# Kernel tuning notes

Hardware: AMD Instinct MI355X
Metric: run time of the kernel (lower is better)

Reference implementation:

```python
import jax, jax.numpy as jnp
import numpy as np
from jax import lax

TAU = 2.0
EPS = 1e-5
STEP = 10      # time steps
RATIO = 4     # TIM_ratio
HEADS = 16
SCALE = 0.25


@jax.custom_vjp
def _spike(v):
    return (v > 0.0).astype(v.dtype)

def _spike_fwd(v):
    return _spike(v), v

def _spike_bwd(v, g):
    alpha = 4.0  # sigmoid surrogate gradient
    s = jax.nn.sigmoid(alpha * v)
    return (g * alpha * s * (1.0 - s),)

_spike.defvjp(_spike_fwd, _spike_bwd)


def lif(x, vth=1.0):
    """LIF neuron over leading time dim: mem += (x-mem)/tau, fire, hard reset (detached)."""
    def step(mem, xt):
        mem = mem + (xt - mem) / TAU
        s = _spike(mem - vth)
        mem = mem * (1.0 - lax.stop_gradient(s))
        return mem, s
    _, out = lax.scan(step, jnp.zeros_like(x[0]), x)
    return out


def bn(x, p, axis):
    """Inference-mode batchnorm; p = stacked (gamma, beta, mean, var) along dim 0."""
    g, b, m, v = p
    sh = [1] * x.ndim
    sh[axis] = -1
    return (x - m.reshape(sh)) / jnp.sqrt(v.reshape(sh) + EPS) * g.reshape(sh) + b.reshape(sh)


def conv3d(x, w, groups=1):
    return lax.conv_general_dilated(
        x, w, window_strides=(1, 1, 1), padding=[(1, 1)] * 3,
        dimension_numbers=('NCDHW', 'OIDHW', 'NCDHW'),
        feature_group_count=groups)


def tim(x, up_w, bn1, down_w, bn2):
    # x: (T, B, C, H, W); conv3d treats T as channels, (C,H,W) as the volume
    T, B, C, H, W = x.shape
    y = conv3d(jnp.swapaxes(x, 0, 1), up_w)                      # (B, T*R, C, H, W)
    y = jnp.swapaxes(bn(y, bn1, 1), 0, 1)                        # (T*R, B, C, H, W)
    # MyNode reshapes (T*R*B, ...) into STEP time chunks of size R*B
    y = lif(y.reshape(STEP, -1, C, H, W)).reshape(T * RATIO, B, C, H, W)
    y = conv3d(jnp.swapaxes(y, 0, 1), down_w, groups=STEP)       # (B, T, C, H, W)
    y = jnp.swapaxes(bn(y, bn2, 1), 0, 1)                        # (T, B, C, H, W)
    return lif(y)


def ssa(x, q_w, q_bn, k_w, k_bn, v_w, v_bn, proj_w, proj_bn,
        tim_up_w, tim_bn1, tim_down_w, tim_bn2):
    T, B, C, H, W = x.shape
    N = H * W
    d = C // HEADS
    xf = x.reshape(T * B, C, N)

    def branch(w, bnp):
        y = bn(jnp.einsum('oc,bcn->bon', w, xf), bnp, 1).reshape(T, B, C, H, W)
        y = tim(y, tim_up_w, tim_bn1, tim_down_w, tim_bn2)       # binary spikes
        y = y.reshape(T, B, C, N).transpose(0, 1, 3, 2)          # (T, B, N, C)
        return y.reshape(T, B, N, HEADS, d).transpose(0, 1, 3, 2, 4)  # (T, B, h, N, d)

    q = branch(q_w, q_bn)
    k = branch(k_w, k_bn)
    v = branch(v_w, v_bn)
    attn = jnp.einsum('tbhnd,tbhmd->tbhnm', q, k)                # no softmax (spiking attn)
    o = jnp.einsum('tbhnm,tbhmd->tbhnd', attn, v) * SCALE
    o = o.transpose(0, 1, 2, 4, 3).reshape(T, B, C, N)           # merge (h, d) -> C
    o = lif(o, vth=0.5)                                          # attn_lif, threshold 0.5
    o = bn(jnp.einsum('oc,tbcn->tbon', proj_w, o), proj_bn, 2)   # 1x1 conv1d + BN1d
    return lif(o).reshape(T, B, C, H, W)


def mlp(x, fc1_w, fc1_b, fc1_bn, fc2_w, fc2_b, fc2_bn):
    T, B, C, H, W = x.shape
    y = jnp.einsum('oc,tbchw->tbohw', fc1_w, x) + fc1_b.reshape(1, 1, -1, 1, 1)
    y = lif(bn(y, fc1_bn, 2))
    y = jnp.einsum('oc,tbchw->tbohw', fc2_w, y) + fc2_b.reshape(1, 1, -1, 1, 1)
    return lif(bn(y, fc2_bn, 2))


def setup_inputs() -> dict:
    key = jax.random.key(0)
    ks = jax.random.split(key, 24)
    T, B, C, H, W = 10, 4, 256, 16, 16
    HID = 1024

    def bnp(k, c):
        k1, k2, k3, k4 = jax.random.split(k, 4)
        gamma = jax.random.uniform(k1, (c,), minval=0.5, maxval=1.5)
        beta = 0.1 * jax.random.normal(k2, (c,))
        mean = 0.1 * jax.random.normal(k3, (c,))
        var = jax.random.uniform(k4, (c,), minval=0.5, maxval=1.5)
        return jnp.stack([gamma, beta, mean, var]).astype(jnp.float32)

    inp = {
        'x': jax.random.normal(ks[0], (T, B, C, H, W), jnp.float32),
        'q_w': jax.random.normal(ks[1], (C, C)) / np.sqrt(C),
        'q_bn': bnp(ks[2], C),
        'k_w': jax.random.normal(ks[3], (C, C)) / np.sqrt(C),
        'k_bn': bnp(ks[4], C),
        'v_w': jax.random.normal(ks[5], (C, C)) / np.sqrt(C),
        'v_bn': bnp(ks[6], C),
        'proj_w': jax.random.normal(ks[7], (C, C)) / np.sqrt(C),
        'proj_bn': bnp(ks[8], C),
        'tim_up_w': jax.random.normal(ks[9], (STEP * RATIO, STEP, 3, 3, 3)) / np.sqrt(STEP * 27),
        'tim_bn1': bnp(ks[10], STEP * RATIO),
        'tim_down_w': jax.random.normal(ks[11], (STEP, RATIO, 3, 3, 3)) / np.sqrt(RATIO * 27),
        'tim_bn2': bnp(ks[12], STEP),
        'fc1_w': jax.random.normal(ks[13], (HID, C)) / np.sqrt(C),
        'fc1_b': 0.1 * jax.random.normal(ks[14], (HID,)),
        'fc1_bn': bnp(ks[15], HID),
        'fc2_w': jax.random.normal(ks[16], (C, HID)) / np.sqrt(HID),
        'fc2_b': 0.1 * jax.random.normal(ks[17], (C,)),
        'fc2_bn': bnp(ks[18], C),
    }
    return {k: v.astype(jnp.float32) for k, v in inp.items()}


def reference(x, q_w, q_bn, k_w, k_bn, v_w, v_bn, proj_w, proj_bn,
              tim_up_w, tim_bn1, tim_down_w, tim_bn2,
              fc1_w, fc1_b, fc1_bn, fc2_w, fc2_b, fc2_bn):
    h = x + ssa(x, q_w, q_bn, k_w, k_bn, v_w, v_bn, proj_w, proj_bn,
                tim_up_w, tim_bn1, tim_down_w, tim_bn2)
    return h + mlp(h, fc1_w, fc1_b, fc1_bn, fc2_w, fc2_b, fc2_bn)
```

## Files before the change

kernel.cpp:

```cpp
#include <hip/hip_runtime.h>
#include <cstdint>
#include <cstddef>

#define EPSF 1e-5f

typedef __attribute__((ext_vector_type(8))) short short8;
typedef __attribute__((ext_vector_type(4))) float f32x4;

__device__ __forceinline__ unsigned short bf16_rne(float f) {
    unsigned int u = __float_as_uint(f);
    u += 0x7FFFu + ((u >> 16) & 1u);
    return (unsigned short)(u >> 16);
}
__device__ __forceinline__ float bf16f(unsigned short h) {
    return __uint_as_float(((unsigned int)h) << 16);
}

__device__ __forceinline__ void split_pack_body(
    const float* __restrict__ W, unsigned short* __restrict__ P,
    int O, int K, int idx)
{
    const int OT = O >> 4, KT = K >> 5;
    const int lane = idx & 63, tile = idx >> 6;
    const int kt = tile % KT, ot = tile / KT;
    const int quad = lane >> 4, l15 = lane & 15;
    const int row = ot * 16 + l15, col = kt * 32 + quad * 8;
    const size_t base = ((size_t)ot * KT + kt) * 512 + lane * 8;
    const size_t sOff = (size_t)OT * KT * 512;
#pragma unroll
    for (int j = 0; j < 8; ++j) {
        float v = W[(size_t)row * K + col + j];
        unsigned short h1 = bf16_rne(v);
        float r = v - bf16f(h1);
        unsigned short h2 = bf16_rne(r);
        float r2 = r - bf16f(h2);
        P[base + j] = h1;
        P[sOff + base + j] = h2;
        P[2 * sOff + base + j] = bf16_rne(r2);
    }
}

__global__ __launch_bounds__(256) void split_pack_k(
    const float* __restrict__ W, unsigned short* __restrict__ P, int O, int K)
{
    int idx = blockIdx.x * 256 + threadIdx.x;
    if (idx >= (O * K) >> 3) return;
    split_pack_body(W, P, O, K, idx);
}

struct SplitArgs { const float* W[3]; unsigned short* P[3]; };
__global__ __launch_bounds__(256) void split_pack3_k(SplitArgs sa, int O, int K)
{
    int idx = blockIdx.x * 256 + threadIdx.x;
    if (idx >= (O * K) >> 3) return;
    split_pack_body(sa.W[blockIdx.y], sa.P[blockIdx.y], O, K, idx);
}

__global__ __launch_bounds__(256) void bpack_k(
    const float* __restrict__ B, unsigned short* __restrict__ BP,
    int K, int N, int S)
{
    const int KT = K >> 5, NT16 = N >> 4;
    int idx = blockIdx.x * 256 + threadIdx.x;
    if (idx >= S * NT16 * KT * 64) return;
    const int lane = idx & 63;
    int tile = idx >> 6;
    const int kt = tile % KT; tile /= KT;
    const int n16 = tile % NT16; const int s = tile / NT16;
    const int quad = lane >> 4, l15 = lane & 15;
    const size_t base = (size_t)idx * 8;
    const size_t sOff = (size_t)S * NT16 * KT * 512;
    const float* src = B + (size_t)s * K * N + (size_t)(kt * 32 + quad * 8) * N
                         + n16 * 16 + l15;
#pragma unroll
    for (int j = 0; j < 8; ++j) {
        float v = src[(size_t)j * N];
        unsigned short h1 = bf16_rne(v);
        float r = v - bf16f(h1);
        unsigned short h2 = bf16_rne(r);
        float r2 = r - bf16f(h2);
        BP[base + j] = h1;
        BP[sOff + base + j] = h2;
        BP[2 * sOff + base + j] = bf16_rne(r2);
    }
}

struct MArgs { const unsigned short* W[3]; float* Out[3]; const float* bn[3]; };

#define MM(AP, BQ)                                                            \
    {                                                                         \
        _Pragma("unroll") for (int mt = 0; mt < 2; ++mt)                      \
        _Pragma("unroll") for (int nt = 0; nt < 2; ++nt)                      \
            acc[mt][nt] = __builtin_amdgcn_mfma_f32_16x16x32_bf16(            \
                Af[AP][mt], Bf[BQ][nt], acc[mt][nt], 0, 0, 0);                \
    }

__global__ __launch_bounds__(256, 4) void mfma_gemm3(
    MArgs a, const unsigned short* __restrict__ BP,
    const float* __restrict__ bias, int O, int K, int N, int nB)
{
    const unsigned short* __restrict__ W = a.W[blockIdx.z];
    float* __restrict__ Out = a.Out[blockIdx.z];
    const float* __restrict__ bnp = a.bn[blockIdx.z];
    const int OT = O >> 4, KT = K >> 5, NT16 = N >> 4;
    const size_t sA = (size_t)OT * KT * 512;
    const size_t sB = (size_t)gridDim.y * NT16 * KT * 512;

    const int slice  = blockIdx.y;
    const int tilesn = N >> 6;
    const int to = (blockIdx.x / tilesn) << 6;
    const int tn = (blockIdx.x % tilesn) << 6;
    const int tid = threadIdx.x;
    const int wid = tid >> 6, lane = tid & 63;
    const int quad = lane >> 4, l15 = lane & 15;
    const int wm = (wid >> 1) << 5, wn = (wid & 1) << 5;
    const int oti0 = (to + wm) >> 4;
    const int n160 = (tn + wn) >> 4;

    f32x4 acc[2][2];
#pragma unroll
    for (int mt = 0; mt < 2; ++mt)
#pragma unroll
        for (int nt = 0; nt < 2; ++nt)
#pragma unroll
            for (int r = 0; r < 4; ++r) acc[mt][nt][r] = 0.0f;

    for (int kt = 0; kt < KT; ++kt) {
        short8 Af[3][2], Bf[3][2];
#pragma unroll
        for (int mt = 0; mt < 2; ++mt) {
            const size_t fa = ((size_t)(oti0 + mt) * KT + kt) * 512 + lane * 8;
            Af[0][mt] = *(const short8*)(W + fa);
            Af[1][mt] = *(const short8*)(W + sA + fa);
            Af[2][mt] = *(const short8*)(W + 2 * sA + fa);
        }
#pragma unroll
        for (int nt = 0; nt < 2; ++nt) {
            const size_t fb =
                (((size_t)slice * NT16 + n160 + nt) * KT + kt) * 512 + lane * 8;
            Bf[0][nt] = *(const short8*)(BP + fb);
            if (nB == 3) {
                Bf[1][nt] = *(const short8*)(BP + sB + fb);
                Bf[2][nt] = *(const short8*)(BP + 2 * sB + fb);
            }
        }
        if (nB == 3) {
            MM(0, 0) MM(0, 1) MM(1, 0) MM(0, 2) MM(1, 1) MM(2, 0)
        } else {
            MM(0, 0) MM(1, 0) MM(2, 0)
        }
    }

    float* Op = Out + (size_t)slice * O * N;
#pragma unroll
    for (int mt = 0; mt < 2; ++mt) {
#pragma unroll
        for (int r = 0; r < 4; ++r) {
            const int o = to + wm + (mt << 4) + (quad << 2) + r;
            float g = bnp[o], bb = bnp[O + o], m = bnp[2 * O + o], vv = bnp[3 * O + o];
            float sq = sqrtf(vv + EPSF);
            float bs = bias ? bias[o] : 0.0f;
#pragma unroll
            for (int nt = 0; nt < 2; ++nt) {
                const int n = tn + wn + (nt << 4) + l15;
                float val = acc[mt][nt][r] + bs;
                Op[(size_t)o * N + n] = (val - m) / sq * g + bb;
            }
        }
    }
}

__global__ __launch_bounds__(256) void wpack6_k(
    const float* __restrict__ up_w, unsigned short* __restrict__ AP)
{
    int idx = blockIdx.x * 256 + threadIdx.x;
    if (idx >= 1920) return;
    const int lane = idx & 63, rest = idx >> 6;
    const int t = rest % 10, mt = rest / 10;
    const int quad = lane >> 4, l15 = lane & 15;
    const int uc = mt * 16 + l15;
    const size_t base = ((size_t)mt * 10 + t) * 512 + lane * 8;
#pragma unroll
    for (int j = 0; j < 8; ++j) {
        int tap = quad * 8 + j;
        float v = 0.0f;
        if (uc < 40 && tap < 27) v = up_w[uc * 270 + t * 27 + tap];
        unsigned short h1 = bf16_rne(v);
        float r = v - bf16f(h1);
        unsigned short h2 = bf16_rne(r);
        float r2 = r - bf16f(h2);
        AP[base + j] = h1;
        AP[15360 + base + j] = h2;
        AP[30720 + base + j] = bf16_rne(r2);
    }
}

struct TimArgs { const float* Y[3]; };

__global__ __launch_bounds__(256, 2) void tim_up6(
    TimArgs ta, const unsigned short* __restrict__ AP,
    const float* __restrict__ bn1, unsigned char* __restrict__ USPK)
{
    __shared__ float smem[12336];
    const float* __restrict__ Y = ta.Y[blockIdx.z];
    unsigned char* __restrict__ SPK = USPK + (size_t)blockIdx.z * 10485760;
    const int c = blockIdx.x, b = blockIdx.y;
    const int tid = threadIdx.x;
    const int wid = tid >> 6, lane = tid & 63;
    const int quad = lane >> 4, l15 = lane & 15;

    int offs[8];
#pragma unroll
    for (int j = 0; j < 8; ++j) {
        int tap = quad * 8 + j;
        if (tap < 27) {
            int kd = tap / 9, rem = tap - kd * 9;
            int kh = rem / 3, kw = rem - kh * 3;
            offs[j] = kd * 360 + kh * 20 + kw;
        } else offs[j] = 0;
    }

    f32x4 acc[3][4];
#pragma unroll
    for (int mt = 0; mt < 3; ++mt)
#pragma unroll
        for (int ng = 0; ng < 4; ++ng)
#pragma unroll
            for (int r = 0; r < 4; ++r) acc[mt][ng][r] = 0.0f;

#pragma unroll 1
    for (int ph = 0; ph < 2; ++ph) {
        __syncthreads();
        for (int idx = tid; idx < 5400; idx += 256) {
            int tt = idx / 1080, rem = idx % 1080;
            int kd = rem / 360, p = rem % 360;
            int row = p / 20, col = p % 20;
            int t = ph * 5 + tt;
            int h = row - 1, ww = col - 1;
            int cs = c + kd - 1;
            float v = 0.0f;
            if (cs >= 0 && cs < 256 && h >= 0 && h < 16 && ww >= 0 && ww < 16)
                v = Y[((t * 4 + b) * 256 + cs) * 256 + h * 16 + ww];
            smem[idx] = v;
        }
        __syncthreads();

#pragma unroll 1
        for (int tt = 0; tt < 5; ++tt) {
            const int t = ph * 5 + tt;
            short8 Af[3][3];
#pragma unroll
            for (int mt = 0; mt < 3; ++mt) {
                const size_t fa = ((size_t)mt * 10 + t) * 512 + lane * 8;
                Af[0][mt] = *(const short8*)(AP + fa);
                Af[1][mt] = *(const short8*)(AP + 15360 + fa);
                Af[2][mt] = *(const short8*)(AP + 30720 + fa);
            }
#pragma unroll
            for (int ng = 0; ng < 4; ++ng) {
                const int base = tt * 1080 + (wid * 4 + ng) * 20 + l15;
                short8 Bf0, Bf1, Bf2;
#pragma unroll
                for (int j = 0; j < 8; ++j) {
                    float v = smem[base + offs[j]];
                    unsigned short h1 = bf16_rne(v);
                    float r = v - bf16f(h1);
                    unsigned short h2 = bf16_rne(r);
                    float r2 = r - bf16f(h2);
                    Bf0[j] = (short)h1;
                    Bf1[j] = (short)h2;
                    Bf2[j] = (short)bf16_rne(r2);
                }
#pragma unroll
                for (int mt = 0; mt < 3; ++mt) {
                    acc[mt][ng] = __builtin_amdgcn_mfma_f32_16x16x32_bf16(
                        Af[0][mt], Bf0, acc[mt][ng], 0, 0, 0);
                    acc[mt][ng] = __builtin_amdgcn_mfma_f32_16x16x32_bf16(
                        Af[0][mt], Bf1, acc[mt][ng], 0, 0, 0);
                    acc[mt][ng] = __builtin_amdgcn_mfma_f32_16x16x32_bf16(
                        Af[1][mt], Bf0, acc[mt][ng], 0, 0, 0);
                    acc[mt][ng] = __builtin_amdgcn_mfma_f32_16x16x32_bf16(
                        Af[0][mt], Bf2, acc[mt][ng], 0, 0, 0);
                    acc[mt][ng] = __builtin_amdgcn_mfma_f32_16x16x32_bf16(
                        Af[1][mt], Bf1, acc[mt][ng], 0, 0, 0);
                    acc[mt][ng] = __builtin_amdgcn_mfma_f32_16x16x32_bf16(
                        Af[2][mt], Bf0, acc[mt][ng], 0, 0, 0);
                }
            }
        }
    }

    __syncthreads();
#pragma unroll
    for (int mt = 0; mt < 3; ++mt)
#pragma unroll
        for (int ng = 0; ng < 4; ++ng)
#pragma unroll
            for (int r = 0; r < 4; ++r) {
                const int uc = mt * 16 + quad * 4 + r;
                const int pix = (wid * 4 + ng) * 16 + l15;
                smem[uc * 257 + pix] = acc[mt][ng][r];
            }
    __syncthreads();

    const int pix = tid;
#pragma unroll
    for (int g = 0; g < 4; ++g) {
        float mem = 0.0f;
#pragma unroll
        for (int s = 0; s < 10; ++s) {
            const int uc = 4 * s + g;
            float ga = bn1[uc], be = bn1[40 + uc], mu = bn1[80 + uc], va = bn1[120 + uc];
            float xv = (smem[uc * 257 + pix] - mu) / sqrtf(va + EPSF) * ga + be;
            mem += (xv - mem) * 0.5f;
            unsigned char spk = mem > 1.0f ? 1 : 0;
            SPK[(((size_t)b * 40 + uc) * 256 + c) * 256 + pix] = spk;
            mem = spk ? 0.0f : mem;
        }
    }
}

struct PtrArgs { float* p[3]; };
struct CPtrArgs { const float* p[3]; };

__global__ __launch_bounds__(256) void tim_down_pre5(
    const unsigned char* __restrict__ USPK, const float* __restrict__ w,
    const float* __restrict__ bn2, PtrArgs PY)
{
    __shared__ float smem[4 * 3 * 324];
    const int br = blockIdx.z / 10, t = blockIdx.z % 10;
    const unsigned char* __restrict__ SPK = USPK + (size_t)br * 10485760;
    float* __restrict__ PreY = PY.p[br];
    const int c = blockIdx.x, b = blockIdx.y;
    const int tid = threadIdx.x;
    for (int idx = tid; idx < 3888; idx += 256) {
        int r = idx / 972, rem = idx % 972;
        int cc = rem / 324, p = rem % 324;
        int hh = p / 18 - 1, ww = p % 18 - 1;
        int cs = c + cc - 1;
        float v = 0.0f;
        if (cs >= 0 && cs < 256 && hh >= 0 && hh < 16 && ww >= 0 && ww < 16)
            v = (float)SPK[(((size_t)b * 40 + 4 * t + r) * 256 + cs) * 256 + hh * 16 + ww];
        smem[idx] = v;
    }
    __syncthreads();
    const int h = tid >> 4, wq = tid & 15;
    float a = 0.0f;
#pragma unroll
    for (int r = 0; r < 4; ++r)
#pragma unroll
        for (int kd = 0; kd < 3; ++kd) {
            const float* wp = w + ((t * 4 + r) * 3 + kd) * 9;
#pragma unroll
            for (int kh = 0; kh < 3; ++kh)
#pragma unroll
                for (int kw = 0; kw < 3; ++kw)
                    a = fmaf(wp[kh * 3 + kw],
                             smem[r * 972 + kd * 324 + (h + kh) * 18 + (wq + kw)], a);
        }
    a = (a - bn2[20 + t]) / sqrtf(bn2[30 + t] + EPSF) * bn2[t] + bn2[10 + t];
    PreY[((t * 4 + b) * 256 + c) * 256 + tid] = a;
}

__global__ __launch_bounds__(256) void lif_down3(CPtrArgs PY, PtrArgs SB)
{
    const float* __restrict__ PreY = PY.p[blockIdx.y];
    float* __restrict__ S = SB.p[blockIdx.y];
    const int idx = blockIdx.x * 256 + threadIdx.x;
    float mem = 0.0f;
    for (int t = 0; t < 10; ++t) {
        float v = PreY[t * 262144 + idx];
        mem += (v - mem) * 0.5f;
        float spk = mem > 1.0f ? 1.0f : 0.0f;
        S[t * 262144 + idx] = spk;
        mem = spk > 0.0f ? 0.0f : mem;
    }
}

__global__ __launch_bounds__(256) void ktv_k(
    const float* __restrict__ SK, const float* __restrict__ SV,
    float* __restrict__ KTV)
{
    __shared__ float ks[16 * 257], vs[16 * 257];
    const int bi = blockIdx.x;
    const int t = bi >> 6, b = (bi >> 4) & 3, hd = bi & 15;
    const int tid = threadIdx.x;
    for (int i = tid; i < 4096; i += 256) {
        int row = i >> 8, col = i & 255;
        ks[row * 257 + col] = SK[((t * 4 + b) * 256 + hd * 16 + row) * 256 + col];
        vs[row * 257 + col] = SV[((t * 4 + b) * 256 + hd * 16 + row) * 256 + col];
    }
    __syncthreads();
    const int j = tid >> 4, j2 = tid & 15;
    float a0 = 0.0f, a1 = 0.0f, a2 = 0.0f, a3 = 0.0f;
#pragma unroll 4
    for (int n = 0; n < 256; n += 4) {
        a0 = fmaf(ks[j * 257 + n + 0], vs[j2 * 257 + n + 0], a0);
        a1 = fmaf(ks[j * 257 + n + 1], vs[j2 * 257 + n + 1], a1);
        a2 = fmaf(ks[j * 257 + n + 2], vs[j2 * 257 + n + 2], a2);
        a3 = fmaf(ks[j * 257 + n + 3], vs[j2 * 257 + n + 3], a3);
    }
    KTV[((t * 4 + b) * 16 + hd) * 256 + tid] = (a0 + a1) + (a2 + a3);
}

__global__ __launch_bounds__(256) void attn_k2(
    const float* __restrict__ SQ, const float* __restrict__ KTV,
    unsigned short* __restrict__ PSPK)
{
    __shared__ float kt[2560];
    __shared__ float qs[16 * 17];
    const int x = blockIdx.x;
    const int b = x >> 8, hd = (x >> 4) & 15, ng = x & 15;
    const int tid = threadIdx.x;
    const int j2 = tid >> 4, nl = tid & 15;
    const int n = ng * 16 + nl;
    for (int i = tid; i < 2560; i += 256) {
        int t = i >> 8;
        kt[i] = KTV[((t * 4 + b) * 16 + hd) * 256 + (i & 255)];
    }
    const int c = hd * 16 + j2;
    const int ktile = c >> 5, quad = (c >> 3) & 3, jj = c & 7;
    const int lane = quad * 16 + nl;
    float mem = 0.0f;
    for (int t = 0; t < 10; ++t) {
        __syncthreads();
        qs[nl * 17 + j2] = SQ[((t * 4 + b) * 256 + hd * 16 + j2) * 256 + n];
        __syncthreads();
        float a = 0.0f;
#pragma unroll
        for (int j = 0; j < 16; ++j)
            a = fmaf(qs[nl * 17 + j], kt[t * 256 + j * 16 + j2], a);
        a *= 0.25f;
        mem += (a - mem) * 0.5f;
        float spk = mem > 0.5f ? 1.0f : 0.0f;
        PSPK[((((size_t)(t * 4 + b) * 16 + ng) * 8 + ktile) * 512) + lane * 8 + jj] =
            spk > 0.0f ? (unsigned short)0x3F80 : (unsigned short)0;
        mem = spk > 0.0f ? 0.0f : mem;
    }
}

__global__ __launch_bounds__(256) void ssa_lif_res(
    const float* __restrict__ P, const float* __restrict__ x,
    float* __restrict__ H)
{
    const int idx = blockIdx.x * 256 + threadIdx.x;
    float mem = 0.0f;
    for (int t = 0; t < 10; ++t) {
        float v = P[t * 262144 + idx];
        mem += (v - mem) * 0.5f;
        float spk = mem > 1.0f ? 1.0f : 0.0f;
        H[t * 262144 + idx] = x[t * 262144 + idx] + spk;
        mem = spk > 0.0f ? 0.0f : mem;
    }
}

__global__ __launch_bounds__(256) void lif_pack(
    const float* __restrict__ A, unsigned short* __restrict__ PB)
{
    const int idx = blockIdx.x * 256 + threadIdx.x;
    const int b = idx >> 18, rem = idx & 262143;
    const int hid = rem >> 8, hw = rem & 255;
    const int ktile = hid >> 5, quad = (hid >> 3) & 3, jj = hid & 7;
    const int n16 = hw >> 4, l15 = hw & 15;
    const int lane = quad * 16 + l15;
    float mem = 0.0f;
    for (int t = 0; t < 10; ++t) {
        float v = A[t * 1048576 + idx];
        mem += (v - mem) * 0.5f;
        float spk = mem > 1.0f ? 1.0f : 0.0f;
        PB[((((size_t)(t * 4 + b) * 16 + n16) * 32 + ktile) * 512) + lane * 8 + jj] =
            spk > 0.0f ? (unsigned short)0x3F80 : (unsigned short)0;
        mem = spk > 0.0f ? 0.0f : mem;
    }
}

__global__ __launch_bounds__(256) void final_k(
    const float* __restrict__ P, const float* __restrict__ H,
    float* __restrict__ out)
{
    const int idx = blockIdx.x * 256 + threadIdx.x;
    float mem = 0.0f;
    for (int t = 0; t < 10; ++t) {
        float v = P[t * 262144 + idx];
        mem += (v - mem) * 0.5f;
        float spk = mem > 1.0f ? 1.0f : 0.0f;
        out[t * 262144 + idx] = H[t * 262144 + idx] + spk;
        mem = spk > 0.0f ? 0.0f : mem;
    }
}

extern "C" void kernel_launch(void* const* d_in, const int* in_sizes, int n_in,
                              void* d_out, int out_size, void* d_ws, size_t ws_size,
                              hipStream_t stream)
{
    const float* x        = (const float*)d_in[0];
    const float* q_w      = (const float*)d_in[1];
    const float* q_bn     = (const float*)d_in[2];
    const float* k_w      = (const float*)d_in[3];
    const float* k_bn     = (const float*)d_in[4];
    const float* v_w      = (const float*)d_in[5];
    const float* v_bn     = (const float*)d_in[6];
    const float* proj_w   = (const float*)d_in[7];
    const float* proj_bn  = (const float*)d_in[8];
    const float* up_w     = (const float*)d_in[9];
    const float* bn1      = (const float*)d_in[10];
    const float* down_w   = (const float*)d_in[11];
    const float* bn2      = (const float*)d_in[12];
    const float* fc1_w    = (const float*)d_in[13];
    const float* fc1_b    = (const float*)d_in[14];
    const float* fc1_bn   = (const float*)d_in[15];
    const float* fc2_w    = (const float*)d_in[16];
    const float* fc2_b    = (const float*)d_in[17];
    const float* fc2_bn   = (const float*)d_in[18];

    float* ws   = (float*)d_ws;
    float* Y    = ws;
    float* ASPK = Y + 2621440;
    float* SQ   = ASPK + 10485760;
    float* SK   = SQ + 2621440;
    float* SV   = SK + 2621440;
    float* KTV  = SV + 2621440;
    unsigned short* AP = (unsigned short*)KTV;

    unsigned short* qs_s = (unsigned short*)ASPK;
    unsigned short* ks_s = qs_s + 196608;
    unsigned short* vs_s = qs_s + 393216;
    unsigned short* xp_s = qs_s + 589824;

    wpack6_k<<<8, 256, 0, stream>>>(up_w, AP);
    SplitArgs sa;
    sa.W[0] = q_w; sa.W[1] = k_w; sa.W[2] = v_w;
    sa.P[0] = qs_s; sa.P[1] = ks_s; sa.P[2] = vs_s;
    split_pack3_k<<<dim3(32, 3), 256, 0, stream>>>(sa, 256, 256);
    bpack_k<<<1280, 256, 0, stream>>>(x, xp_s, 256, 256, 40);

    MArgs qkv;
    qkv.W[0] = qs_s;  qkv.W[1] = ks_s;  qkv.W[2] = vs_s;
    qkv.Out[0] = Y; qkv.Out[1] = SK; qkv.Out[2] = SV;
    qkv.bn[0] = q_bn; qkv.bn[1] = k_bn; qkv.bn[2] = v_bn;
    mfma_gemm3<<<dim3(16, 40, 3), 256, 0, stream>>>(qkv, xp_s, nullptr, 256, 256, 256, 3);

    unsigned char* USPK = (unsigned char*)ASPK;
    TimArgs ta; ta.Y[0] = Y; ta.Y[1] = SK; ta.Y[2] = SV;
    tim_up6<<<dim3(256, 4, 3), 256, 0, stream>>>(ta, AP, bn1, USPK);

    PtrArgs PY; PY.p[0] = Y; PY.p[1] = SK; PY.p[2] = SV;
    tim_down_pre5<<<dim3(256, 4, 30), 256, 0, stream>>>(USPK, down_w, bn2, PY);

    CPtrArgs PYc; PYc.p[0] = Y; PYc.p[1] = SK; PYc.p[2] = SV;
    PtrArgs SB; SB.p[0] = SQ; SB.p[1] = SK; SB.p[2] = SV;
    lif_down3<<<dim3(1024, 3), 256, 0, stream>>>(PYc, SB);

    ktv_k<<<640, 256, 0, stream>>>(SK, SV, KTV);
    unsigned short* PSPK = (unsigned short*)Y;
    attn_k2<<<1024, 256, 0, stream>>>(SQ, KTV, PSPK);

    unsigned short* pj_s = (unsigned short*)ASPK;
    split_pack_k<<<32, 256, 0, stream>>>(proj_w, pj_s, 256, 256);
    MArgs gp; gp.W[0] = gp.W[1] = gp.W[2] = pj_s;
    gp.Out[0] = gp.Out[1] = gp.Out[2] = SQ;
    gp.bn[0] = gp.bn[1] = gp.bn[2] = proj_bn;
    mfma_gemm3<<<dim3(16, 40, 1), 256, 0, stream>>>(gp, PSPK, nullptr, 256, 256, 256, 1);
    ssa_lif_res<<<1024, 256, 0, stream>>>(SQ, x, SV);

    unsigned short* f1b = (unsigned short*)SQ;
    bpack_k<<<1280, 256, 0, stream>>>(SV, f1b, 256, 256, 40);
    unsigned short* f1_s = (unsigned short*)Y;
    split_pack_k<<<128, 256, 0, stream>>>(fc1_w, f1_s, 1024, 256);
    MArgs g1; g1.W[0] = g1.W[1] = g1.W[2] = f1_s;
    g1.Out[0] = g1.Out[1] = g1.Out[2] = ASPK;
    g1.bn[0] = g1.bn[1] = g1.bn[2] = fc1_bn;
    mfma_gemm3<<<dim3(64, 40, 1), 256, 0, stream>>>(g1, f1b, fc1_b, 1024, 256, 256, 3);

    unsigned short* PB2 = (unsigned short*)SQ;
    lif_pack<<<4096, 256, 0, stream>>>(ASPK, PB2);
    unsigned short* f2_s = (unsigned short*)Y;
    split_pack_k<<<128, 256, 0, stream>>>(fc2_w, f2_s, 256, 1024);
    MArgs g2; g2.W[0] = g2.W[1] = g2.W[2] = f2_s;
    g2.Out[0] = g2.Out[1] = g2.Out[2] = ASPK;
    g2.bn[0] = g2.bn[1] = g2.bn[2] = fc2_bn;
    mfma_gemm3<<<dim3(16, 40, 1), 256, 0, stream>>>(g2, PB2, fc2_b, 256, 1024, 256, 1);
    final_k<<<1024, 256, 0, stream>>>(ASPK, SV, (float*)d_out);
}
```

Before: 673.0 us.

## Pre-split input to bf16 triples in shared memory and halve LDS footprint

The tim_up kernel now splits each input value into three bf16 parts once, while staging it into shared memory. Previously the split was redone for every tap inside the MFMA loop. Shared memory is cut from about 48KB to about 32KB, and the accumulator spill to LDS for the BN+LIF epilogue is done in two chunks carrying membrane state between them. Launch bounds move from 2 to 4 blocks per SM to raise occupancy. The trade-offs are extra register pressure under the tighter bound and an additional sync and store phase in the epilogue.

```diff
diff --git a/kernel.cpp b/kernel.cpp
--- a/kernel.cpp
+++ b/kernel.cpp
@@ -197,11 +197,13 @@
 
 struct TimArgs { const float* Y[3]; };
 
-__global__ __launch_bounds__(256, 2) void tim_up6(
+__global__ __launch_bounds__(256, 4) void tim_up8(
     TimArgs ta, const unsigned short* __restrict__ AP,
     const float* __restrict__ bn1, unsigned char* __restrict__ USPK)
 {
-    __shared__ float smem[12336];
+    __shared__ float smem[8100];
+    unsigned short* smemA = (unsigned short*)smem;
+    unsigned short* smemB = smemA + 10800;
     const float* __restrict__ Y = ta.Y[blockIdx.z];
     unsigned char* __restrict__ SPK = USPK + (size_t)blockIdx.z * 10485760;
     const int c = blockIdx.x, b = blockIdx.y;
@@ -241,7 +243,13 @@
             float v = 0.0f;
             if (cs >= 0 && cs < 256 && h >= 0 && h < 16 && ww >= 0 && ww < 16)
                 v = Y[((t * 4 + b) * 256 + cs) * 256 + h * 16 + ww];
-            smem[idx] = v;
+            unsigned short h1 = bf16_rne(v);
+            float r = v - bf16f(h1);
+            unsigned short h2 = bf16_rne(r);
+            float r2 = r - bf16f(h2);
+            *(unsigned int*)&smemA[idx * 2] =
+                (unsigned int)h1 | ((unsigned int)h2 << 16);
+            smemB[idx] = bf16_rne(r2);
         }
         __syncthreads();
 
@@ -262,14 +270,11 @@
                 short8 Bf0, Bf1, Bf2;
 #pragma unroll
                 for (int j = 0; j < 8; ++j) {
-                    float v = smem[base + offs[j]];
-                    unsigned short h1 = bf16_rne(v);
-                    float r = v - bf16f(h1);
-                    unsigned short h2 = bf16_rne(r);
-                    float r2 = r - bf16f(h2);
-                    Bf0[j] = (short)h1;
-                    Bf1[j] = (short)h2;
-                    Bf2[j] = (short)bf16_rne(r2);
+                    unsigned int p01 =
+                        *(const unsigned int*)&smemA[(base + offs[j]) * 2];
+                    Bf0[j] = (short)(p01 & 0xFFFFu);
+                    Bf1[j] = (short)(p01 >> 16);
+                    Bf2[j] = (short)smemB[base + offs[j]];
                 }
 #pragma unroll
                 for (int mt = 0; mt < 3; ++mt) {
@@ -290,6 +295,9 @@
         }
     }
 
+    const int pix = tid;
+    float memv[4] = {0.0f, 0.0f, 0.0f, 0.0f};
+
     __syncthreads();
 #pragma unroll
     for (int mt = 0; mt < 3; ++mt)
@@ -298,20 +306,46 @@
 #pragma unroll
             for (int r = 0; r < 4; ++r) {
                 const int uc = mt * 16 + quad * 4 + r;
-                const int pix = (wid * 4 + ng) * 16 + l15;
-                smem[uc * 257 + pix] = acc[mt][ng][r];
+                if (uc < 24)
+                    smem[uc * 257 + (wid * 4 + ng) * 16 + l15] = acc[mt][ng][r];
             }
     __syncthreads();
-
-    const int pix = tid;
 #pragma unroll
     for (int g = 0; g < 4; ++g) {
-        float mem = 0.0f;
-#pragma unroll
-        for (int s = 0; s < 10; ++s) {
+        float mem = memv[g];
+#pragma unroll
+        for (int s = 0; s < 6; ++s) {
             const int uc = 4 * s + g;
             float ga = bn1[uc], be = bn1[40 + uc], mu = bn1[80 + uc], va = bn1[120 + uc];
             float xv = (smem[uc * 257 + pix] - mu) / sqrtf(va + EPSF) * ga + be;
+            mem += (xv - mem) * 0.5f;
+            unsigned char spk = mem > 1.0f ? 1 : 0;
+            SPK[(((size_t)b * 40 + uc) * 256 + c) * 256 + pix] = spk;
+            mem = spk ? 0.0f : mem;
+        }
+        memv[g] = mem;
+    }
+
+    __syncthreads();
+#pragma unroll
+    for (int mt = 1; mt < 3; ++mt)
+#pragma unroll
+        for (int ng = 0; ng < 4; ++ng)
+#pragma unroll
+            for (int r = 0; r < 4; ++r) {
+                const int uc = mt * 16 + quad * 4 + r;
+                if (uc >= 24)
+                    smem[(uc - 24) * 257 + (wid * 4 + ng) * 16 + l15] = acc[mt][ng][r];
+            }
+    __syncthreads();
+#pragma unroll
+    for (int g = 0; g < 4; ++g) {
+        float mem = memv[g];
+#pragma unroll
+        for (int s = 6; s < 10; ++s) {
+            const int uc = 4 * s + g;
+            float ga = bn1[uc], be = bn1[40 + uc], mu = bn1[80 + uc], va = bn1[120 + uc];
+            float xv = (smem[(uc - 24) * 257 + pix] - mu) / sqrtf(va + EPSF) * ga + be;
             mem += (xv - mem) * 0.5f;
             unsigned char spk = mem > 1.0f ? 1 : 0;
             SPK[(((size_t)b * 40 + uc) * 256 + c) * 256 + pix] = spk;
@@ -542,7 +576,7 @@
 
     unsigned char* USPK = (unsigned char*)ASPK;
     TimArgs ta; ta.Y[0] = Y; ta.Y[1] = SK; ta.Y[2] = SV;
-    tim_up6<<<dim3(256, 4, 3), 256, 0, stream>>>(ta, AP, bn1, USPK);
+    tim_up8<<<dim3(256, 4, 3), 256, 0, stream>>>(ta, AP, bn1, USPK);
 
     PtrArgs PY; PY.p[0] = Y; PY.p[1] = SK; PY.p[2] = SV;
     tim_down_pre5<<<dim3(256, 4, 30), 256, 0, stream>>>(USPK, down_w, bn2, PY);
```

After: 791.6 us. +17.6%, slower.
